# Kernel tuning notes

Measured on AMD Instinct MI355X. Metric: run time of the kernel, lower is better.

Reference implementation:

```python
import jax, jax.numpy as jnp
import numpy as np

N_NODES = 65536
N_EDGES = 524288
IN_CH = 128
HEADS = 4
HID = 16          # per-head channels (hidden_channels)
HC = HEADS * HID  # 64
EDGE_F = 8
N_GRAPHS = 512


def _glorot(key, shape):
    return jax.random.normal(key, shape, dtype=jnp.float32) / np.float32(np.sqrt(shape[0]))


def setup_inputs() -> dict:
    key = jax.random.key(0)
    ks = jax.random.split(key, 16)
    inp = {}
    inp['x'] = jax.random.normal(ks[0], (N_NODES, IN_CH), jnp.float32)
    inp['edge_attr'] = jax.random.normal(ks[1], (N_EDGES, EDGE_F), jnp.float32)
    inp['edge_index'] = jax.random.randint(ks[2], (2, N_EDGES), 0, N_NODES, dtype=jnp.int32)
    inp['batch'] = jnp.sort(jax.random.randint(ks[3], (N_NODES,), 0, N_GRAPHS, dtype=jnp.int32))
    fan1 = {'Wq1': IN_CH, 'Wk1': IN_CH, 'Wv1': IN_CH, 'We1': EDGE_F, 'Ws1': IN_CH}
    fan2 = {'Wq2': HC, 'Wk2': HC, 'Wv2': HC, 'We2': EDGE_F, 'Ws2': HC}
    i = 4
    for name, fi in {**fan1, **fan2}.items():
        inp[name] = _glorot(ks[i], (fi, HC)); i += 1
    for b in ['bq1', 'bk1', 'bv1', 'be1', 'bs1', 'bq2', 'bk2', 'bv2', 'be2', 'bs2']:
        inp[b] = jnp.zeros((HC,), jnp.float32)
    return inp


def _tconv(x, src, dst, ea, Wq, Wk, Wv, We, Ws, bq, bk, bv, be, bs):
    """PyG TransformerConv (concat=True, root_weight=True), eval mode (no dropout)."""
    n = x.shape[0]
    q = (x @ Wq + bq).reshape(n, HEADS, HID)[dst]      # [E,H,C] query at target
    k = (x @ Wk + bk).reshape(n, HEADS, HID)[src]      # [E,H,C] key from source
    v = (x @ Wv + bv).reshape(n, HEADS, HID)[src]      # [E,H,C]
    e = (ea @ We + be).reshape(-1, HEADS, HID)         # [E,H,C] edge proj
    k = k + e
    logits = (q * k).sum(-1) / np.float32(np.sqrt(HID))  # [E,H]
    m = jax.ops.segment_max(logits, dst, num_segments=n)
    m = jnp.where(jnp.isfinite(m), m, jnp.zeros_like(m))
    a = jnp.exp(logits - m[dst])
    denom = jax.ops.segment_sum(a, dst, num_segments=n)
    alpha = a / jnp.maximum(denom[dst], 1e-16)         # segment softmax over incoming edges
    msg = (v + e) * alpha[..., None]                   # [E,H,C]
    out = jax.ops.segment_sum(msg, dst, num_segments=n).reshape(n, HC)
    return out + x @ Ws + bs                           # root/skip connection


def reference(x, edge_attr, Wq1, Wk1, Wv1, We1, Ws1, bq1, bk1, bv1, be1, bs1,
              Wq2, Wk2, Wv2, We2, Ws2, bq2, bk2, bv2, be2, bs2,
              edge_index, batch):
    src, dst = edge_index[0], edge_index[1]
    h = jax.nn.relu(_tconv(x, src, dst, edge_attr,
                           Wq1, Wk1, Wv1, We1, Ws1, bq1, bk1, bv1, be1, bs1))
    h = _tconv(h, src, dst, edge_attr,
               Wq2, Wk2, Wv2, We2, Ws2, bq2, bk2, bv2, be2, bs2)
    # mean_pool_nodes: segment mean per graph
    sums = jax.ops.segment_sum(h, batch, num_segments=N_GRAPHS)
    counts = jax.ops.segment_sum(jnp.ones((h.shape[0], 1), h.dtype), batch, num_segments=N_GRAPHS)
    return sums / jnp.maximum(counts, 1.0)
```

## Files before the change

kernel.cpp:

```cpp
#include <hip/hip_runtime.h>
#include <hip/hip_bf16.h>
#include <math.h>

#define N_NODES 65536
#define N_EDGES 524288
#define IN_CH 128
#define HC 64
#define N_GRAPHS 512
#define BUCKET_CAP 64

typedef __attribute__((ext_vector_type(8))) short short8v;
typedef __attribute__((ext_vector_type(4))) float float4v;

__device__ __forceinline__ ushort f32_to_bf16_rne(float x) {
    unsigned u = __float_as_uint(x);
    return (ushort)((u + 0x7fffu + ((u >> 16) & 1u)) >> 16);
}
__device__ __forceinline__ float bf16_to_f32(ushort h) {
    return __uint_as_float(((unsigned)h) << 16);
}

__global__ void build_buckets(const int* __restrict__ ei, int* __restrict__ cnt,
                              int2* __restrict__ bucket) {
    int e = blockIdx.x * 256 + threadIdx.x;
    if (e >= N_EDGES) return;
    int s = ei[e];
    int d = ei[N_EDGES + e];
    int pos = atomicAdd(&cnt[d], 1);
    if (pos < BUCKET_CAP) bucket[d * BUCKET_CAP + pos] = make_int2(e, s);
}

__global__ void pack_weights(
    const float* __restrict__ Wq1, const float* __restrict__ Wk1,
    const float* __restrict__ Wv1, const float* __restrict__ Ws1,
    const float* __restrict__ Wq2, const float* __restrict__ Wk2,
    const float* __restrict__ Wv2, const float* __restrict__ Ws2,
    ushort* __restrict__ wf1_hi, ushort* __restrict__ wf1_lo,
    ushort* __restrict__ wf2_hi, ushort* __restrict__ wf2_lo) {
    int f = blockIdx.x * 256 + threadIdx.x;
    if (f >= 6144) return;
    const float* W;
    ushort *ph, *pl;
    int fl;
    if (f < 4096) {
        int mat = f >> 10; fl = f & 1023;
        W = (mat == 0) ? Wq1 : (mat == 1) ? Wk1 : (mat == 2) ? Wv1 : Ws1;
        ph = wf1_hi + (size_t)mat * 1024 * 8;
        pl = wf1_lo + (size_t)mat * 1024 * 8;
    } else {
        int g = f - 4096;
        int mat = g >> 9; fl = g & 511;
        W = (mat == 0) ? Wq2 : (mat == 1) ? Wk2 : (mat == 2) ? Wv2 : Ws2;
        ph = wf2_hi + (size_t)mat * 512 * 8;
        pl = wf2_lo + (size_t)mat * 512 * 8;
    }
    int lane = fl & 63;
    int ct = (fl >> 6) & 3;
    int ks = fl >> 8;
    int col = ct * 16 + (lane & 15);
    int k0 = ks * 32 + (lane >> 4) * 8;
    ushort h8[8], l8[8];
#pragma unroll
    for (int j = 0; j < 8; ++j) {
        float w = W[(size_t)(k0 + j) * HC + col];
        ushort h = f32_to_bf16_rne(w);
        float r = w - bf16_to_f32(h);
        h8[j] = h;
        l8[j] = f32_to_bf16_rne(r);
    }
    *(uint4*)&ph[(size_t)fl * 8] = *(uint4*)h8;
    *(uint4*)&pl[(size_t)fl * 8] = *(uint4*)l8;
}

template <int FIN>
__global__ __launch_bounds__(256, 2) void node_gemm_mfma(
    const float* __restrict__ xin,
    const ushort* __restrict__ wf_hi, const ushort* __restrict__ wf_lo,
    const float* __restrict__ bq, const float* __restrict__ bk,
    const float* __restrict__ bv, const float* __restrict__ bs,
    float* __restrict__ q, float* __restrict__ kv, float* __restrict__ hout) {
    constexpr int NPB = 128;
    constexpr int KS = FIN / 32;
    constexpr int KC = FIN / 8;
    __shared__ ushort xs[2 * NPB * KC * 8];
    constexpr int LOHALF = NPB * KC * 8;
    const int tid = threadIdx.x;
    const int lane = tid & 63;
    const int w = tid >> 6;
    const int n0 = blockIdx.x * NPB;

    for (int c = tid; c < NPB * KC; c += 256) {
        int r = c / KC, kc = c % KC;
        const float4* src = (const float4*)(xin + (size_t)(n0 + r) * FIN + kc * 8);
        float4 x0 = src[0], x1 = src[1];
        float xv[8] = {x0.x, x0.y, x0.z, x0.w, x1.x, x1.y, x1.z, x1.w};
        ushort h[8], l[8];
#pragma unroll
        for (int j = 0; j < 8; ++j) {
            h[j] = f32_to_bf16_rne(xv[j]);
            l[j] = f32_to_bf16_rne(xv[j] - bf16_to_f32(h[j]));
        }
        int kcs = kc ^ (r & 7);
        *(uint4*)&xs[(size_t)(r * KC + kcs) * 8] = *(uint4*)h;
        *(uint4*)&xs[LOHALF + (size_t)(r * KC + kcs) * 8] = *(uint4*)l;
    }

    const int ch16 = lane & 15;
    float bqv[4], bkv[4], bvv[4], bsv[4];
#pragma unroll
    for (int ct = 0; ct < 4; ++ct) {
        bqv[ct] = bq[ct * 16 + ch16];
        bkv[ct] = bk[ct * 16 + ch16];
        bvv[ct] = bv[ct * 16 + ch16];
        bsv[ct] = bs[ct * 16 + ch16];
    }
    float4v acc[2][16];
#pragma unroll
    for (int t = 0; t < 16; ++t) {
        int mat = t >> 2, ct = t & 3;
        float b = (mat == 0) ? bqv[ct] : (mat == 1) ? bkv[ct]
                : (mat == 2) ? bvv[ct] : bsv[ct];
        acc[0][t] = (float4v){b, b, b, b};
        acc[1][t] = (float4v){b, b, b, b};
    }
    __syncthreads();

    const int g = lane >> 4;
    for (int ks = 0; ks < KS; ++ks) {
        short8v ah[2], al[2];
#pragma unroll
        for (int mt = 0; mt < 2; ++mt) {
            int r = w * 32 + mt * 16 + (lane & 15);
            int kcs = (ks * 4 + g) ^ (r & 7);
            ah[mt] = *(const short8v*)&xs[(size_t)(r * KC + kcs) * 8];
            al[mt] = *(const short8v*)&xs[LOHALF + (size_t)(r * KC + kcs) * 8];
        }
#pragma unroll
        for (int t = 0; t < 16; ++t) {
            int mat = t >> 2, ct = t & 3;
            size_t fo = (((size_t)mat * KS * 4) + ks * 4 + ct) * 64 + lane;
            short8v bh = *(const short8v*)&wf_hi[fo * 8];
            short8v bl = *(const short8v*)&wf_lo[fo * 8];
            acc[0][t] = __builtin_amdgcn_mfma_f32_16x16x32_bf16(ah[0], bh, acc[0][t], 0, 0, 0);
            acc[1][t] = __builtin_amdgcn_mfma_f32_16x16x32_bf16(ah[1], bh, acc[1][t], 0, 0, 0);
            acc[0][t] = __builtin_amdgcn_mfma_f32_16x16x32_bf16(al[0], bh, acc[0][t], 0, 0, 0);
            acc[1][t] = __builtin_amdgcn_mfma_f32_16x16x32_bf16(al[1], bh, acc[1][t], 0, 0, 0);
            acc[0][t] = __builtin_amdgcn_mfma_f32_16x16x32_bf16(ah[0], bl, acc[0][t], 0, 0, 0);
            acc[1][t] = __builtin_amdgcn_mfma_f32_16x16x32_bf16(ah[1], bl, acc[1][t], 0, 0, 0);
        }
    }

    const int rloc = (lane >> 4) * 4;
#pragma unroll
    for (int mt = 0; mt < 2; ++mt) {
        int nbase = n0 + w * 32 + mt * 16 + rloc;
#pragma unroll
        for (int t = 0; t < 16; ++t) {
            int mat = t >> 2;
            int ch = (t & 3) * 16 + ch16;
#pragma unroll
            for (int r2 = 0; r2 < 4; ++r2) {
                int n = nbase + r2;
                float v = acc[mt][t][r2];
                if (mat == 0)      q[(size_t)n * HC + ch] = v;
                else if (mat == 1) kv[(size_t)n * 128 + ch] = v;
                else if (mat == 2) kv[(size_t)n * 128 + 64 + ch] = v;
                else               hout[(size_t)n * HC + ch] = v;
            }
        }
    }
}

__device__ __forceinline__ float dpp_sum16(float x) {
    int t;
    t = __builtin_amdgcn_update_dpp(0, __float_as_int(x), 0xB1, 0xF, 0xF, true);
    x += __int_as_float(t);
    t = __builtin_amdgcn_update_dpp(0, __float_as_int(x), 0x4E, 0xF, 0xF, true);
    x += __int_as_float(t);
    t = __builtin_amdgcn_update_dpp(0, __float_as_int(x), 0x141, 0xF, 0xF, true);
    x += __int_as_float(t);
    t = __builtin_amdgcn_update_dpp(0, __float_as_int(x), 0x140, 0xF, 0xF, true);
    x += __int_as_float(t);
    return x;
}

template <int RELU>
__global__ __launch_bounds__(256) void aggregate(
    const float* __restrict__ q, const float* __restrict__ kv,
    const float* __restrict__ ea,
    const float* __restrict__ We, const float* __restrict__ be,
    const int* __restrict__ cnt,
    const int2* __restrict__ bucket, float* __restrict__ hout) {
    const int wave = threadIdx.x >> 6;
    const int c = threadIdx.x & 63;
    const int n = blockIdx.x * 4 + wave;

    const float qc = q[n * HC + c] * 0.25f;
    int deg = cnt[n];
    if (deg > BUCKET_CAP) deg = BUCKET_CAP;

    int myeid = 0, mysrc = 0;
    if (c < deg) {
        int2 b = bucket[n * BUCKET_CAP + c];
        myeid = b.x;
        mysrc = b.y;
    }

    const float bec = be[c];
    float wec[8];
#pragma unroll
    for (int f = 0; f < 8; ++f) wec[f] = We[f * HC + c];

    float m = -INFINITY, d = 0.f, o = 0.f;

    float4 eA0, eA1, eB0, eB1, nA0, nA1, nB0, nB1;
    float kA, vA, kB, vB, nkA, nvA, nkB, nvB;

#define LOAD_EDGE(idx, E0, E1, KC, VC)                                   \
    {                                                                    \
        int eid_ = __builtin_amdgcn_readlane(myeid, (idx));              \
        int s_   = __builtin_amdgcn_readlane(mysrc, (idx));              \
        E0 = *(const float4*)(ea + (size_t)eid_ * 8);                    \
        E1 = *(const float4*)(ea + (size_t)eid_ * 8 + 4);                \
        KC = kv[(size_t)s_ * 128 + c];                                   \
        VC = kv[(size_t)s_ * 128 + 64 + c];                              \
    }

#define EDGE_PROJ(E0, E1, EC)                                            \
    float EC = bec;                                                      \
    EC = fmaf(E0.x, wec[0], EC); EC = fmaf(E0.y, wec[1], EC);            \
    EC = fmaf(E0.z, wec[2], EC); EC = fmaf(E0.w, wec[3], EC);            \
    EC = fmaf(E1.x, wec[4], EC); EC = fmaf(E1.y, wec[5], EC);            \
    EC = fmaf(E1.z, wec[6], EC); EC = fmaf(E1.w, wec[7], EC);

    const int npairs = deg >> 1;

    if (deg >= 2) {
        LOAD_EDGE(0, eA0, eA1, kA, vA);
        LOAD_EDGE(1, eB0, eB1, kB, vB);
    } else if (deg == 1) {
        LOAD_EDGE(0, eA0, eA1, kA, vA);
    }

    for (int p = 0; p < npairs; ++p) {
        int base = (p + 1) * 2;
        if (base + 1 < deg) {
            LOAD_EDGE(base, nA0, nA1, nkA, nvA);
            LOAD_EDGE(base + 1, nB0, nB1, nkB, nvB);
        } else if (base < deg) {
            LOAD_EDGE(base, nA0, nA1, nkA, nvA);
        }

        EDGE_PROJ(eA0, eA1, ecA);
        EDGE_PROJ(eB0, eB1, ecB);

        float pA = dpp_sum16(qc * (kA + ecA));
        float pB = dpp_sum16(qc * (kB + ecB));

        float newm = fmaxf(m, fmaxf(pA, pB));
        float scale = __expf(m - newm);
        float wA = __expf(pA - newm);
        float wB = __expf(pB - newm);
        d = d * scale + wA + wB;
        o = o * scale + (vA + ecA) * wA + (vB + ecB) * wB;
        m = newm;

        eA0 = nA0; eA1 = nA1; kA = nkA; vA = nvA;
        eB0 = nB0; eB1 = nB1; kB = nkB; vB = nvB;
    }

    if (deg & 1) {
        EDGE_PROJ(eA0, eA1, ecA);
        float pA = dpp_sum16(qc * (kA + ecA));
        float newm = fmaxf(m, pA);
        float scale = __expf(m - newm);
        float wA = __expf(pA - newm);
        d = d * scale + wA;
        o = o * scale + (vA + ecA) * wA;
    }

#undef LOAD_EDGE
#undef EDGE_PROJ

    float msg = (deg > 0) ? (o / d) : 0.f;
    float val = hout[n * HC + c] + msg;
    if (RELU) val = fmaxf(val, 0.f);
    hout[n * HC + c] = val;
}

__device__ __forceinline__ int lower_bound(const int* __restrict__ b, int val) {
    int lo = 0, hi = N_NODES;
    while (lo < hi) {
        int mid = (lo + hi) >> 1;
        if (b[mid] < val) lo = mid + 1; else hi = mid;
    }
    return lo;
}

__global__ __launch_bounds__(256) void pool_graph(const float* __restrict__ h,
                                                  const int* __restrict__ batch,
                                                  float* __restrict__ out) {
    const int g = blockIdx.x * 4 + (threadIdx.x >> 6);
    const int c = threadIdx.x & 63;
    const int s = lower_bound(batch, g);
    const int e = lower_bound(batch, g + 1);

    float a0 = 0.f, a1 = 0.f, a2 = 0.f, a3 = 0.f;
    int i = s;
    for (; i + 4 <= e; i += 4) {
        a0 += h[(size_t)i * HC + c];
        a1 += h[(size_t)(i + 1) * HC + c];
        a2 += h[(size_t)(i + 2) * HC + c];
        a3 += h[(size_t)(i + 3) * HC + c];
    }
    for (; i < e; ++i) a0 += h[(size_t)i * HC + c];
    float acc = (a0 + a1) + (a2 + a3);
    out[g * HC + c] = acc / fmaxf((float)(e - s), 1.f);
}

extern "C" void kernel_launch(void* const* d_in, const int* in_sizes, int n_in,
                              void* d_out, int out_size, void* d_ws, size_t ws_size,
                              hipStream_t stream) {
    const float* x     = (const float*)d_in[0];
    const float* ea    = (const float*)d_in[1];
    const int*   ei    = (const int*)d_in[2];
    const int*   batch = (const int*)d_in[3];
    const float* Wq1 = (const float*)d_in[4];
    const float* Wk1 = (const float*)d_in[5];
    const float* Wv1 = (const float*)d_in[6];
    const float* We1 = (const float*)d_in[7];
    const float* Ws1 = (const float*)d_in[8];
    const float* Wq2 = (const float*)d_in[9];
    const float* Wk2 = (const float*)d_in[10];
    const float* Wv2 = (const float*)d_in[11];
    const float* We2 = (const float*)d_in[12];
    const float* Ws2 = (const float*)d_in[13];
    const float* bq1 = (const float*)d_in[14];
    const float* bk1 = (const float*)d_in[15];
    const float* bv1 = (const float*)d_in[16];
    const float* be1 = (const float*)d_in[17];
    const float* bs1 = (const float*)d_in[18];
    const float* bq2 = (const float*)d_in[19];
    const float* bk2 = (const float*)d_in[20];
    const float* bv2 = (const float*)d_in[21];
    const float* be2 = (const float*)d_in[22];
    const float* bs2 = (const float*)d_in[23];
    float* out = (float*)d_out;

    char* ws = (char*)d_ws;
    size_t off = 0;
    auto alloc = [&](size_t bytes) -> void* {
        void* p = ws + off;
        off += (bytes + 255) & ~(size_t)255;
        return p;
    };
    int*    cnt    = (int*)alloc((size_t)N_NODES * 4);
    int2*   bucket = (int2*)alloc((size_t)N_NODES * BUCKET_CAP * 8);
    float*  q      = (float*)alloc((size_t)N_NODES * HC * 4);
    float*  kv     = (float*)alloc((size_t)N_NODES * 128 * 4);
    float*  h1     = (float*)alloc((size_t)N_NODES * HC * 4);
    float*  h2     = (float*)alloc((size_t)N_NODES * HC * 4);
    ushort* wf1_hi = (ushort*)alloc((size_t)4 * 1024 * 8 * 2);
    ushort* wf1_lo = (ushort*)alloc((size_t)4 * 1024 * 8 * 2);
    ushort* wf2_hi = (ushort*)alloc((size_t)4 * 512 * 8 * 2);
    ushort* wf2_lo = (ushort*)alloc((size_t)4 * 512 * 8 * 2);

    hipMemsetAsync(cnt, 0, (size_t)N_NODES * 4, stream);
    build_buckets<<<N_EDGES / 256, 256, 0, stream>>>(ei, cnt, bucket);
    pack_weights<<<24, 256, 0, stream>>>(Wq1, Wk1, Wv1, Ws1, Wq2, Wk2, Wv2, Ws2,
                                         wf1_hi, wf1_lo, wf2_hi, wf2_lo);

    node_gemm_mfma<IN_CH><<<N_NODES / 128, 256, 0, stream>>>(
        x, wf1_hi, wf1_lo, bq1, bk1, bv1, bs1, q, kv, h1);
    aggregate<1><<<N_NODES / 4, 256, 0, stream>>>(
        q, kv, ea, We1, be1, cnt, bucket, h1);

    node_gemm_mfma<HC><<<N_NODES / 128, 256, 0, stream>>>(
        h1, wf2_hi, wf2_lo, bq2, bk2, bv2, bs2, q, kv, h2);
    aggregate<0><<<N_NODES / 4, 256, 0, stream>>>(
        q, kv, ea, We2, be2, cnt, bucket, h2);

    pool_graph<<<N_GRAPHS / 4, 256, 0, stream>>>(h2, batch, out);
}
```

Measured before the change: 325.8 us.

## Store edge attributes inline in dst buckets and interleave K/V per channel

```diff
diff --git a/kernel.cpp b/kernel.cpp
--- a/kernel.cpp
+++ b/kernel.cpp
@@ -7,7 +7,7 @@
 #define IN_CH 128
 #define HC 64
 #define N_GRAPHS 512
-#define BUCKET_CAP 64
+#define BUCKET_CAP 32
 
 typedef __attribute__((ext_vector_type(8))) short short8v;
 typedef __attribute__((ext_vector_type(4))) float float4v;
@@ -20,14 +20,30 @@
     return __uint_as_float(((unsigned)h) << 16);
 }
 
-__global__ void build_buckets(const int* __restrict__ ei, int* __restrict__ cnt,
-                              int2* __restrict__ bucket) {
+struct __align__(16) BEntry {
+    float4 ea0;
+    float4 ea1;
+    int src;
+    int pad[3];
+};
+
+__global__ void build_buckets(const int* __restrict__ ei,
+                              const float* __restrict__ ea,
+                              int* __restrict__ cnt,
+                              BEntry* __restrict__ bucket) {
     int e = blockIdx.x * 256 + threadIdx.x;
     if (e >= N_EDGES) return;
     int s = ei[e];
     int d = ei[N_EDGES + e];
+    float4 a0 = *(const float4*)(ea + (size_t)e * 8);
+    float4 a1 = *(const float4*)(ea + (size_t)e * 8 + 4);
     int pos = atomicAdd(&cnt[d], 1);
-    if (pos < BUCKET_CAP) bucket[d * BUCKET_CAP + pos] = make_int2(e, s);
+    if (pos < BUCKET_CAP) {
+        BEntry* be = &bucket[(size_t)d * BUCKET_CAP + pos];
+        be->ea0 = a0;
+        be->ea1 = a1;
+        be->src = s;
+    }
 }
 
 __global__ void pack_weights(
@@ -155,17 +171,15 @@
     for (int mt = 0; mt < 2; ++mt) {
         int nbase = n0 + w * 32 + mt * 16 + rloc;
 #pragma unroll
-        for (int t = 0; t < 16; ++t) {
-            int mat = t >> 2;
-            int ch = (t & 3) * 16 + ch16;
+        for (int ct = 0; ct < 4; ++ct) {
+            int ch = ct * 16 + ch16;
 #pragma unroll
             for (int r2 = 0; r2 < 4; ++r2) {
                 int n = nbase + r2;
-                float v = acc[mt][t][r2];
-                if (mat == 0)      q[(size_t)n * HC + ch] = v;
-                else if (mat == 1) kv[(size_t)n * 128 + ch] = v;
-                else if (mat == 2) kv[(size_t)n * 128 + 64 + ch] = v;
-                else               hout[(size_t)n * HC + ch] = v;
+                q[(size_t)n * HC + ch] = acc[mt][ct][r2];
+                *(float2*)&kv[(size_t)n * 128 + 2 * ch] =
+                    make_float2(acc[mt][4 + ct][r2], acc[mt][8 + ct][r2]);
+                hout[(size_t)n * HC + ch] = acc[mt][12 + ct][r2];
             }
         }
     }
@@ -187,10 +201,9 @@
 template <int RELU>
 __global__ __launch_bounds__(256) void aggregate(
     const float* __restrict__ q, const float* __restrict__ kv,
-    const float* __restrict__ ea,
     const float* __restrict__ We, const float* __restrict__ be,
     const int* __restrict__ cnt,
-    const int2* __restrict__ bucket, float* __restrict__ hout) {
+    const BEntry* __restrict__ bucket, float* __restrict__ hout) {
     const int wave = threadIdx.x >> 6;
     const int c = threadIdx.x & 63;
     const int n = blockIdx.x * 4 + wave;
@@ -199,12 +212,10 @@
     int deg = cnt[n];
     if (deg > BUCKET_CAP) deg = BUCKET_CAP;
 
-    int myeid = 0, mysrc = 0;
-    if (c < deg) {
-        int2 b = bucket[n * BUCKET_CAP + c];
-        myeid = b.x;
-        mysrc = b.y;
-    }
+    const BEntry* bkt = bucket + (size_t)n * BUCKET_CAP;
+
+    int mysrc = 0;
+    if (c < deg) mysrc = bkt[c].src;
 
     const float bec = be[c];
     float wec[8];
@@ -214,16 +225,15 @@
     float m = -INFINITY, d = 0.f, o = 0.f;
 
     float4 eA0, eA1, eB0, eB1, nA0, nA1, nB0, nB1;
-    float kA, vA, kB, vB, nkA, nvA, nkB, nvB;
-
-#define LOAD_EDGE(idx, E0, E1, KC, VC)                                   \
+    float2 kvA, kvB, nkvA, nkvB;
+
+#define LOAD_EDGE(idx, E0, E1, KV)                                       \
     {                                                                    \
-        int eid_ = __builtin_amdgcn_readlane(myeid, (idx));              \
-        int s_   = __builtin_amdgcn_readlane(mysrc, (idx));              \
-        E0 = *(const float4*)(ea + (size_t)eid_ * 8);                    \
-        E1 = *(const float4*)(ea + (size_t)eid_ * 8 + 4);                \
-        KC = kv[(size_t)s_ * 128 + c];                                   \
-        VC = kv[(size_t)s_ * 128 + 64 + c];                              \
+        int s_ = __builtin_amdgcn_readlane(mysrc, (idx));                \
+        const BEntry* be_ = bkt + (idx);                                 \
+        E0 = be_->ea0;                                                   \
+        E1 = be_->ea1;                                                   \
+        KV = *(const float2*)&kv[(size_t)s_ * 128 + 2 * c];              \
     }
 
 #define EDGE_PROJ(E0, E1, EC)                                            \
@@ -236,47 +246,47 @@
     const int npairs = deg >> 1;
 
     if (deg >= 2) {
-        LOAD_EDGE(0, eA0, eA1, kA, vA);
-        LOAD_EDGE(1, eB0, eB1, kB, vB);
+        LOAD_EDGE(0, eA0, eA1, kvA);
+        LOAD_EDGE(1, eB0, eB1, kvB);
     } else if (deg == 1) {
-        LOAD_EDGE(0, eA0, eA1, kA, vA);
+        LOAD_EDGE(0, eA0, eA1, kvA);
     }
 
     for (int p = 0; p < npairs; ++p) {
         int base = (p + 1) * 2;
         if (base + 1 < deg) {
-            LOAD_EDGE(base, nA0, nA1, nkA, nvA);
-            LOAD_EDGE(base + 1, nB0, nB1, nkB, nvB);
+            LOAD_EDGE(base, nA0, nA1, nkvA);
+            LOAD_EDGE(base + 1, nB0, nB1, nkvB);
         } else if (base < deg) {
-            LOAD_EDGE(base, nA0, nA1, nkA, nvA);
+            LOAD_EDGE(base, nA0, nA1, nkvA);
         }
 
         EDGE_PROJ(eA0, eA1, ecA);
         EDGE_PROJ(eB0, eB1, ecB);
 
-        float pA = dpp_sum16(qc * (kA + ecA));
-        float pB = dpp_sum16(qc * (kB + ecB));
+        float pA = dpp_sum16(qc * (kvA.x + ecA));
+        float pB = dpp_sum16(qc * (kvB.x + ecB));
 
         float newm = fmaxf(m, fmaxf(pA, pB));
         float scale = __expf(m - newm);
         float wA = __expf(pA - newm);
         float wB = __expf(pB - newm);
         d = d * scale + wA + wB;
-        o = o * scale + (vA + ecA) * wA + (vB + ecB) * wB;
+        o = o * scale + (kvA.y + ecA) * wA + (kvB.y + ecB) * wB;
         m = newm;
 
-        eA0 = nA0; eA1 = nA1; kA = nkA; vA = nvA;
-        eB0 = nB0; eB1 = nB1; kB = nkB; vB = nvB;
+        eA0 = nA0; eA1 = nA1; kvA = nkvA;
+        eB0 = nB0; eB1 = nB1; kvB = nkvB;
     }
 
     if (deg & 1) {
         EDGE_PROJ(eA0, eA1, ecA);
-        float pA = dpp_sum16(qc * (kA + ecA));
+        float pA = dpp_sum16(qc * (kvA.x + ecA));
         float newm = fmaxf(m, pA);
         float scale = __expf(m - newm);
         float wA = __expf(pA - newm);
         d = d * scale + wA;
-        o = o * scale + (vA + ecA) * wA;
+        o = o * scale + (kvA.y + ecA) * wA;
     }
 
 #undef LOAD_EDGE
@@ -355,7 +365,7 @@
         return p;
     };
     int*    cnt    = (int*)alloc((size_t)N_NODES * 4);
-    int2*   bucket = (int2*)alloc((size_t)N_NODES * BUCKET_CAP * 8);
+    BEntry* bucket = (BEntry*)alloc((size_t)N_NODES * BUCKET_CAP * sizeof(BEntry));
     float*  q      = (float*)alloc((size_t)N_NODES * HC * 4);
     float*  kv     = (float*)alloc((size_t)N_NODES * 128 * 4);
     float*  h1     = (float*)alloc((size_t)N_NODES * HC * 4);
@@ -366,19 +376,19 @@
     ushort* wf2_lo = (ushort*)alloc((size_t)4 * 512 * 8 * 2);
 
     hipMemsetAsync(cnt, 0, (size_t)N_NODES * 4, stream);
-    build_buckets<<<N_EDGES / 256, 256, 0, stream>>>(ei, cnt, bucket);
+    build_buckets<<<N_EDGES / 256, 256, 0, stream>>>(ei, ea, cnt, bucket);
     pack_weights<<<24, 256, 0, stream>>>(Wq1, Wk1, Wv1, Ws1, Wq2, Wk2, Wv2, Ws2,
                                          wf1_hi, wf1_lo, wf2_hi, wf2_lo);
 
     node_gemm_mfma<IN_CH><<<N_NODES / 128, 256, 0, stream>>>(
         x, wf1_hi, wf1_lo, bq1, bk1, bv1, bs1, q, kv, h1);
     aggregate<1><<<N_NODES / 4, 256, 0, stream>>>(
-        q, kv, ea, We1, be1, cnt, bucket, h1);
+        q, kv, We1, be1, cnt, bucket, h1);
 
     node_gemm_mfma<HC><<<N_NODES / 128, 256, 0, stream>>>(
         h1, wf2_hi, wf2_lo, bq2, bk2, bv2, bs2, q, kv, h2);
     aggregate<0><<<N_NODES / 4, 256, 0, stream>>>(
-        q, kv, ea, We2, be2, cnt, bucket, h2);
+        q, kv, We2, be2, cnt, bucket, h2);
 
     pool_graph<<<N_GRAPHS / 4, 256, 0, stream>>>(h2, batch, out);
 }
```

After: 352.4 us. 8.2% more time.
